# Performance work log

Hardware: AMD Instinct MI355X
Metric: run time of the kernel (lower is better)

## Reference

```python
import jax, jax.numpy as jnp
import numpy as np

B, N, D = 4, 1024, 512
H, Dv, Dq = 8, 64, 64
NUM_BUCKETS = 64
LN_EPS = 1e-5


def setup_inputs() -> dict:
    key = jax.random.key(0)
    ks = jax.random.split(key, 10)
    x = jax.random.normal(ks[0], (B, N, D), dtype=jnp.float32)
    ts = jnp.sort(jax.random.randint(ks[1], (B, N), 0, 1_000_000), axis=1).astype(jnp.int64)
    cm = jnp.triu(jnp.ones((N, N), dtype=bool), k=1)  # causal: mask j > i
    pm = jnp.zeros((B, N), dtype=bool)                # no padding
    uvqk = 0.02 * jax.random.normal(ks[2], (D, 2 * H * Dv + 2 * H * Dq), dtype=jnp.float32)
    lim = float(np.sqrt(6.0 / (H * Dv + D)))
    o_w = jax.random.uniform(ks[3], (H * Dv, D), minval=-lim, maxval=lim, dtype=jnp.float32)
    o_b = jnp.zeros((D,), dtype=jnp.float32)
    ln_x_w = jnp.ones((D,), jnp.float32); ln_x_b = jnp.zeros((D,), jnp.float32)
    ln_a_w = jnp.ones((H * Dv,), jnp.float32); ln_a_b = jnp.zeros((H * Dv,), jnp.float32)
    ts_w = 0.02 * jax.random.normal(ks[4], (NUM_BUCKETS + 1,), dtype=jnp.float32)
    pos_w = 0.02 * jax.random.normal(ks[5], (2 * N - 1,), dtype=jnp.float32)
    return {"x": x, "ts": ts, "cm": cm, "pm": pm, "uvqk": uvqk, "o_w": o_w, "o_b": o_b,
            "ln_x_w": ln_x_w, "ln_x_b": ln_x_b, "ln_a_w": ln_a_w, "ln_a_b": ln_a_b,
            "ts_w": ts_w, "pos_w": pos_w}


def _layernorm(x, w, b):
    m = jnp.mean(x, axis=-1, keepdims=True)
    v = jnp.mean(jnp.square(x - m), axis=-1, keepdims=True)
    return (x - m) / jnp.sqrt(v + LN_EPS) * w + b


def _rel_bias(ts, ts_w, pos_w):
    # positional part: pb[i, j] = pos_w[j - i + N - 1], shape [N, N]
    idx = jnp.arange(N)
    pb = pos_w[idx[None, :] - idx[:, None] + N - 1]
    # bucketed time part
    ext = jnp.concatenate([ts, ts[:, N - 1:N]], axis=1)           # [B, N+1]
    diff = ext[:, 1:, None] - ext[:, None, :-1]                   # [B, N, N]
    logd = jnp.log(jnp.maximum(jnp.abs(diff), 1).astype(jnp.float32))
    bk = jnp.clip((logd / 0.301).astype(jnp.int32), 0, NUM_BUCKETS)
    return pb[None] + ts_w[bk]                                    # [B, N, N]


def reference(x, ts, cm, pm, uvqk, o_w, o_b, ln_x_w, ln_x_b, ln_a_w, ln_a_b, ts_w, pos_w):
    nx = _layernorm(x, ln_x_w, ln_x_b)                            # [B, N, D]
    out = jax.nn.silu(jnp.einsum('bnd,de->bne', nx, uvqk))        # [B, N, 2HDv+2HDq]
    u, v, q, k = jnp.split(out, [H * Dv, 2 * H * Dv, 2 * H * Dv + H * Dq], axis=-1)
    q = q.reshape(B, N, H, Dq)
    k = k.reshape(B, N, H, Dq)
    v = v.reshape(B, N, H, Dv)
    qk = jnp.einsum('bihd,bjhd->bhij', q, k) + _rel_bias(ts, ts_w, pos_w)[:, None]
    qk = jax.nn.silu(qk) / N
    qk = jnp.where(cm[None, None], 0.0, qk)          # causal mask
    qk = jnp.where(pm[:, None, None, :], 0.0, qk)    # padding mask on keys
    ao = jnp.einsum('bhij,bjhd->bihd', qk, v).reshape(B, N, H * Dv)
    ao = _layernorm(ao, ln_a_w, ln_a_b)
    u = u.reshape(B, N, H * Dv)
    y = (u * ao) @ o_w + o_b + x
    return jnp.where(pm[:, :, None], 0.0, y)
```

## Files before the change

kernel.cpp:

```cpp
#include <hip/hip_runtime.h>


typedef __attribute__((ext_vector_type(8))) short short8;
typedef __attribute__((ext_vector_type(4))) short bf4;
typedef __attribute__((ext_vector_type(4))) float floatx4;

#define MFMA_BF16 __builtin_amdgcn_mfma_f32_16x16x32_bf16

static __device__ __forceinline__ short f2bf(float f) {
  unsigned u = __builtin_bit_cast(unsigned, f);
  u = (u + 0x7fffu + ((u >> 16) & 1u)) >> 16;
  return (short)u;
}
static __device__ __forceinline__ float bf2f(short s) {
  unsigned u = ((unsigned)(unsigned short)s) << 16;
  return __builtin_bit_cast(float, u);
}
static __device__ __forceinline__ float silu_f(float x) {
  return x / (1.f + __expf(-x));
}
static __device__ __forceinline__ void gl_lds16(const void* g, void* l) {
  __builtin_amdgcn_global_load_lds(
      (const __attribute__((address_space(1))) unsigned int*)g,
      (__attribute__((address_space(3))) unsigned int*)l, 16, 0, 0);
}

__global__ __launch_bounds__(256) void prep_kernel(
    const float* __restrict__ x, const int* __restrict__ ts,
    const float* __restrict__ uvqk, const float* __restrict__ o_w,
    const float* __restrict__ ln_x_w, const float* __restrict__ ln_x_b,
    const float* __restrict__ ts_w, const float* __restrict__ pos_w,
    short* __restrict__ nx, short* __restrict__ uvqk_t,
    short* __restrict__ o_wt, short* __restrict__ bias) {
  __shared__ float tile[32][33];
  const int id = blockIdx.x;
  const int t = threadIdx.x;
  if (id < 4096) {
    const int b = id >> 10, i = id & 1023;
    int ie = i + 1; if (ie > 1023) ie = 1023;
    const int tse = ts[(b << 10) + ie];
    const int j0 = t * 4;
    int4 tj = *(const int4*)&ts[(b << 10) + j0];
    const int* tjp = (const int*)&tj;
    bf4 o;
#pragma unroll
    for (int e = 0; e < 4; ++e) {
      int dt = tse - tjp[e];
      float ad = fabsf((float)dt);
      if (ad < 1.f) ad = 1.f;
      int bkt = (int)(__logf(ad) * (1.f / 0.301f));
      if (bkt > 64) bkt = 64;
      o[e] = f2bf(pos_w[j0 + e - i + 1023] + ts_w[bkt]);
    }
    *(bf4*)&bias[((size_t)id << 10) + j0] = o;
  } else if (id < 5120) {
    const int lane = t & 63;
    const int row = ((id - 4096) << 2) + (t >> 6);
    const int c0 = lane * 8;
    const float* xr = x + (size_t)row * 512;
    float v[8];
    *(float4*)&v[0] = *(const float4*)(xr + c0);
    *(float4*)&v[4] = *(const float4*)(xr + c0 + 4);
    float s = 0.f, sq = 0.f;
#pragma unroll
    for (int e = 0; e < 8; ++e) { s += v[e]; sq += v[e] * v[e]; }
#pragma unroll
    for (int off = 32; off > 0; off >>= 1) {
      s += __shfl_xor(s, off);
      sq += __shfl_xor(sq, off);
    }
    float m = s * (1.f / 512.f);
    float var = sq * (1.f / 512.f) - m * m;
    float rinv = rsqrtf(var + 1e-5f);
    float wv[8], bv[8];
    *(float4*)&wv[0] = *(const float4*)(ln_x_w + c0);
    *(float4*)&wv[4] = *(const float4*)(ln_x_w + c0 + 4);
    *(float4*)&bv[0] = *(const float4*)(ln_x_b + c0);
    *(float4*)&bv[4] = *(const float4*)(ln_x_b + c0 + 4);
    short8 o;
#pragma unroll
    for (int e = 0; e < 8; ++e) o[e] = f2bf((v[e] - m) * rinv * wv[e] + bv[e]);
    *(short8*)(nx + (size_t)row * 512 + c0) = o;
  } else {
    const float* src; short* dst; int R, C, bc, br;
    if (id < 6144) {
      int idm = id - 5120;
      src = uvqk; dst = uvqk_t; R = 512; C = 2048;
      bc = (idm & 63) * 32; br = (idm >> 6) * 32;
    } else {
      int idm = id - 6144;
      src = o_w; dst = o_wt; R = 512; C = 512;
      bc = (idm & 15) * 32; br = (idm >> 4) * 32;
    }
    const int c = t & 31, r0 = t >> 5;
#pragma unroll
    for (int p = 0; p < 4; ++p) {
      int r = r0 + p * 8;
      tile[r][c] = src[(size_t)(br + r) * C + bc + c];
    }
    __syncthreads();
#pragma unroll
    for (int p = 0; p < 4; ++p) {
      int r = r0 + p * 8;
      dst[(size_t)(bc + r) * R + br + c] = f2bf(tile[c][r]);
    }
  }
}

__global__ __launch_bounds__(256) void gemm1_kernel(
    const short* __restrict__ A, const short* __restrict__ Bt,
    short* __restrict__ u_buf, short* __restrict__ vt_buf,
    short* __restrict__ q_buf, short* __restrict__ k_buf) {
  __shared__ __align__(16) short As[2][128 * 32];
  __shared__ __align__(16) short Bs[2][128 * 32];
  const int t = threadIdx.x;
  const int lane = t & 63, w = t >> 6;
  const int quad = lane >> 4, l15 = lane & 15;
  const int m0 = blockIdx.x * 128, n0 = blockIdx.y * 128;
  const int wm = (w & 1) * 64, wn = (w >> 1) * 64;
  const int lr = lane >> 2, lc = (lane & 3) * 8;
  floatx4 acc[4][4];
#pragma unroll
  for (int i = 0; i < 4; ++i)
#pragma unroll
    for (int j = 0; j < 4; ++j) acc[i][j] = (floatx4){0.f, 0.f, 0.f, 0.f};

  for (int k0 = 0; k0 < 512; k0 += 64) {
    __syncthreads();
#pragma unroll
    for (int c = 0; c < 2; ++c)
#pragma unroll
      for (int p = 0; p < 2; ++p) {
        int ra = w * 32 + p * 16;
        gl_lds16(&A[(size_t)(m0 + ra + lr) * 512 + k0 + c * 32 + lc], &As[c][ra * 32]);
        gl_lds16(&Bt[(size_t)(n0 + ra + lr) * 512 + k0 + c * 32 + lc], &Bs[c][ra * 32]);
      }
    __syncthreads();
#pragma unroll
    for (int c = 0; c < 2; ++c) {
      short8 af[4], bfr[4];
#pragma unroll
      for (int mi = 0; mi < 4; ++mi) af[mi] = *(const short8*)&As[c][(wm + mi * 16 + l15) * 32 + quad * 8];
#pragma unroll
      for (int ni = 0; ni < 4; ++ni) bfr[ni] = *(const short8*)&Bs[c][(wn + ni * 16 + l15) * 32 + quad * 8];
#pragma unroll
      for (int mi = 0; mi < 4; ++mi)
#pragma unroll
        for (int ni = 0; ni < 4; ++ni)
          acc[mi][ni] = MFMA_BF16(af[mi], bfr[ni], acc[mi][ni], 0, 0, 0);
    }
  }
  const int seg = n0 >> 9, cbase = n0 & 511;
  if (seg == 0) {
#pragma unroll
    for (int mi = 0; mi < 4; ++mi)
#pragma unroll
      for (int ni = 0; ni < 4; ++ni)
#pragma unroll
        for (int r = 0; r < 4; ++r) {
          int row = m0 + wm + mi * 16 + quad * 4 + r;
          int c = cbase + wn + ni * 16 + l15;
          u_buf[(size_t)row * 512 + c] = f2bf(silu_f(acc[mi][ni][r]));
        }
  } else if (seg == 1) {
#pragma unroll
    for (int mi = 0; mi < 4; ++mi)
#pragma unroll
      for (int ni = 0; ni < 4; ++ni) {
        int c = cbase + wn + ni * 16 + l15;
        int h = c >> 6, d = c & 63;
        int row0 = m0 + wm + mi * 16 + quad * 4;
        int b_ = row0 >> 10, nb = row0 & 1023;
        bf4 sv;
#pragma unroll
        for (int r = 0; r < 4; ++r) sv[r] = f2bf(silu_f(acc[mi][ni][r]));
        *(bf4*)&vt_buf[(((size_t)(b_ * 8 + h) * 64 + d) << 10) + nb] = sv;
      }
  } else {
    short* dst = (seg == 2) ? q_buf : k_buf;
#pragma unroll
    for (int mi = 0; mi < 4; ++mi)
#pragma unroll
      for (int ni = 0; ni < 4; ++ni)
#pragma unroll
        for (int r = 0; r < 4; ++r) {
          int row = m0 + wm + mi * 16 + quad * 4 + r;
          int c = cbase + wn + ni * 16 + l15;
          int b_ = row >> 10, nseq = row & 1023;
          size_t idx = ((((size_t)(b_ * 8 + (c >> 6))) << 10) + nseq) * 64 + (c & 63);
          dst[idx] = f2bf(silu_f(acc[mi][ni][r]));
        }
  }
}

__global__ __launch_bounds__(256, 4) void attn_kernel(
    const short* __restrict__ q_buf, const short* __restrict__ k_buf,
    const short* __restrict__ vt_buf, const short* __restrict__ bias_buf,
    short* __restrict__ ao_part) {
  __shared__ __align__(16) short q_s[64][72];
  __shared__ __align__(16) short k_s[64][72];
  __shared__ __align__(16) short vt_s[64][72];
  __shared__ __align__(16) short p_s[64][72];

  const int t = threadIdx.x;
  const int lane = t & 63, w = t >> 6;
  const int quad = lane >> 4, l15 = lane & 15;
  const int bh = blockIdx.x, pair = blockIdx.y, jh = blockIdx.z;
  const int b = bh >> 3, h = bh & 7;
  const short* qh = q_buf + (size_t)bh * 65536;
  const short* kh = k_buf + (size_t)bh * 65536;
  const short* vth = vt_buf + (size_t)bh * 65536;
  const int sr = t >> 2, sc = (t & 3) * 16;

#pragma unroll
  for (int half = 0; half < 2; ++half) {
    const int it = half ? (15 - pair) : pair;
    const int i0 = it * 64;
    {
      float4 qr0 = *(const float4*)&qh[(size_t)(i0 + sr) * 64 + sc];
      float4 qr1 = *(const float4*)&qh[(size_t)(i0 + sr) * 64 + sc + 8];
      *(float4*)&q_s[sr][sc] = qr0;
      *(float4*)&q_s[sr][sc + 8] = qr1;
    }
    float4 kr0, kr1, vr0, vr1;
    if (jh <= it) {
      int j0 = jh * 64;
      kr0 = *(const float4*)&kh[(size_t)(j0 + sr) * 64 + sc];
      kr1 = *(const float4*)&kh[(size_t)(j0 + sr) * 64 + sc + 8];
      vr0 = *(const float4*)&vth[(size_t)sr * 1024 + j0 + sc];
      vr1 = *(const float4*)&vth[(size_t)sr * 1024 + j0 + sc + 8];
    }
    floatx4 ao0 = {0.f, 0.f, 0.f, 0.f}, ao1 = ao0, ao2 = ao0, ao3 = ao0;
    for (int jt = jh; jt <= it; jt += 4) {
      const int j0 = jt * 64;
      short br[4][4];
      {
        const short* bb = &bias_buf[((size_t)(b * 1024 + i0 + w * 16 + quad * 4) << 10) + j0 + l15];
#pragma unroll
        for (int ni = 0; ni < 4; ++ni)
#pragma unroll
          for (int r2 = 0; r2 < 4; ++r2)
            br[ni][r2] = bb[((size_t)r2 << 10) + ni * 16];
      }
      __syncthreads();
      *(float4*)&k_s[sr][sc] = kr0;
      *(float4*)&k_s[sr][sc + 8] = kr1;
      *(float4*)&vt_s[sr][sc] = vr0;
      *(float4*)&vt_s[sr][sc + 8] = vr1;
      {
        int jn = (jt + 4 <= it) ? jt + 4 : jt;
        int jn0 = jn * 64;
        kr0 = *(const float4*)&kh[(size_t)(jn0 + sr) * 64 + sc];
        kr1 = *(const float4*)&kh[(size_t)(jn0 + sr) * 64 + sc + 8];
        vr0 = *(const float4*)&vth[(size_t)sr * 1024 + jn0 + sc];
        vr1 = *(const float4*)&vth[(size_t)sr * 1024 + jn0 + sc + 8];
      }
      __syncthreads();
      floatx4 s0 = {0.f, 0.f, 0.f, 0.f}, s1 = s0, s2 = s0, s3 = s0;
#pragma unroll
      for (int kk = 0; kk < 64; kk += 32) {
        short8 aq = *(const short8*)&q_s[w * 16 + l15][kk + quad * 8];
        s0 = MFMA_BF16(aq, *(const short8*)&k_s[0 + l15][kk + quad * 8], s0, 0, 0, 0);
        s1 = MFMA_BF16(aq, *(const short8*)&k_s[16 + l15][kk + quad * 8], s1, 0, 0, 0);
        s2 = MFMA_BF16(aq, *(const short8*)&k_s[32 + l15][kk + quad * 8], s2, 0, 0, 0);
        s3 = MFMA_BF16(aq, *(const short8*)&k_s[48 + l15][kk + quad * 8], s3, 0, 0, 0);
      }
      const bool diag = (jt == it);
      floatx4 sv[4] = {s0, s1, s2, s3};
#pragma unroll
      for (int ni = 0; ni < 4; ++ni) {
        int j_loc = ni * 16 + l15;
#pragma unroll
        for (int r2 = 0; r2 < 4; ++r2) {
          int i_loc = w * 16 + quad * 4 + r2;
          float xx = sv[ni][r2] + bf2f(br[ni][r2]);
          float pv = silu_f(xx) * (1.f / 1024.f);
          if (diag && j_loc > i_loc) pv = 0.f;
          p_s[i_loc][j_loc] = f2bf(pv);
        }
      }
#pragma unroll
      for (int kk = 0; kk < 64; kk += 32) {
        short8 ap = *(const short8*)&p_s[w * 16 + l15][kk + quad * 8];
        ao0 = MFMA_BF16(ap, *(const short8*)&vt_s[0 + l15][kk + quad * 8], ao0, 0, 0, 0);
        ao1 = MFMA_BF16(ap, *(const short8*)&vt_s[16 + l15][kk + quad * 8], ao1, 0, 0, 0);
        ao2 = MFMA_BF16(ap, *(const short8*)&vt_s[32 + l15][kk + quad * 8], ao2, 0, 0, 0);
        ao3 = MFMA_BF16(ap, *(const short8*)&vt_s[48 + l15][kk + quad * 8], ao3, 0, 0, 0);
      }
    }
    floatx4 aov[4] = {ao0, ao1, ao2, ao3};
    short* aod = ao_part + (size_t)jh * 2097152;
#pragma unroll
    for (int ni = 0; ni < 4; ++ni)
#pragma unroll
      for (int r2 = 0; r2 < 4; ++r2) {
        int gi = i0 + w * 16 + quad * 4 + r2;
        int d = ni * 16 + l15;
        aod[((size_t)(b * 1024 + gi)) * 512 + h * 64 + d] = f2bf(aov[ni][r2]);
      }
  }
}

__global__ __launch_bounds__(256) void ln_mul_kernel(
    const short* __restrict__ ao_part, const short* __restrict__ u,
    const float* __restrict__ w_, const float* __restrict__ b_,
    short* __restrict__ g) {
  const int lane = threadIdx.x & 63;
  const int row = (blockIdx.x << 2) + (threadIdx.x >> 6);
  const int c0 = lane * 8;
  short8 a0 = *(const short8*)(ao_part + (size_t)row * 512 + c0);
  short8 a1 = *(const short8*)(ao_part + 2097152 + (size_t)row * 512 + c0);
  short8 a2 = *(const short8*)(ao_part + 4194304 + (size_t)row * 512 + c0);
  short8 a3 = *(const short8*)(ao_part + 6291456 + (size_t)row * 512 + c0);
  float v[8];
#pragma unroll
  for (int e = 0; e < 8; ++e)
    v[e] = (bf2f(a0[e]) + bf2f(a1[e])) + (bf2f(a2[e]) + bf2f(a3[e]));
  float s = 0.f, sq = 0.f;
#pragma unroll
  for (int e = 0; e < 8; ++e) { s += v[e]; sq += v[e] * v[e]; }
#pragma unroll
  for (int off = 32; off > 0; off >>= 1) {
    s += __shfl_xor(s, off);
    sq += __shfl_xor(sq, off);
  }
  float m = s * (1.f / 512.f);
  float var = sq * (1.f / 512.f) - m * m;
  float rinv = rsqrtf(var + 1e-5f);
  float wv[8], bv[8];
  *(float4*)&wv[0] = *(const float4*)(w_ + c0);
  *(float4*)&wv[4] = *(const float4*)(w_ + c0 + 4);
  *(float4*)&bv[0] = *(const float4*)(b_ + c0);
  *(float4*)&bv[4] = *(const float4*)(b_ + c0 + 4);
  short8 uv = *(const short8*)(u + (size_t)row * 512 + c0);
  short8 o;
#pragma unroll
  for (int e = 0; e < 8; ++e)
    o[e] = f2bf(bf2f(uv[e]) * ((v[e] - m) * rinv * wv[e] + bv[e]));
  *(short8*)(g + (size_t)row * 512 + c0) = o;
}

__global__ __launch_bounds__(256) void gemm2_kernel(
    const short* __restrict__ G, const short* __restrict__ Wt,
    const float* __restrict__ o_b, const float* __restrict__ x,
    float* __restrict__ out) {
  __shared__ __align__(16) short As[2][64 * 32];
  __shared__ __align__(16) short Bs[2][64 * 32];
  const int t = threadIdx.x;
  const int lane = t & 63, w = t >> 6;
  const int quad = lane >> 4, l15 = lane & 15;
  const int m0 = blockIdx.x * 64, n0 = blockIdx.y * 64;
  const int lr = lane >> 2, lc = (lane & 3) * 8;
  floatx4 acc[4];
#pragma unroll
  for (int j = 0; j < 4; ++j) acc[j] = (floatx4){0.f, 0.f, 0.f, 0.f};

  for (int k0 = 0; k0 < 512; k0 += 64) {
    __syncthreads();
#pragma unroll
    for (int c = 0; c < 2; ++c) {
      int ra = w * 16;
      gl_lds16(&G[(size_t)(m0 + ra + lr) * 512 + k0 + c * 32 + lc], &As[c][ra * 32]);
      gl_lds16(&Wt[(size_t)(n0 + ra + lr) * 512 + k0 + c * 32 + lc], &Bs[c][ra * 32]);
    }
    __syncthreads();
#pragma unroll
    for (int c = 0; c < 2; ++c) {
      short8 af = *(const short8*)&As[c][(w * 16 + l15) * 32 + quad * 8];
#pragma unroll
      for (int ni = 0; ni < 4; ++ni) {
        short8 bfr = *(const short8*)&Bs[c][(ni * 16 + l15) * 32 + quad * 8];
        acc[ni] = MFMA_BF16(af, bfr, acc[ni], 0, 0, 0);
      }
    }
  }
#pragma unroll
  for (int ni = 0; ni < 4; ++ni)
#pragma unroll
    for (int r = 0; r < 4; ++r) {
      int row = m0 + w * 16 + quad * 4 + r;
      int c = n0 + ni * 16 + l15;
      out[(size_t)row * 512 + c] = acc[ni][r] + o_b[c] + x[(size_t)row * 512 + c];
    }
}

extern "C" void kernel_launch(void* const* d_in, const int* in_sizes, int n_in,
                              void* d_out, int out_size, void* d_ws, size_t ws_size,
                              hipStream_t stream) {
  const float* x = (const float*)d_in[0];
  const int* ts = (const int*)d_in[1];
  const float* uvqk = (const float*)d_in[4];
  const float* o_w = (const float*)d_in[5];
  const float* o_b = (const float*)d_in[6];
  const float* ln_x_w = (const float*)d_in[7];
  const float* ln_x_b = (const float*)d_in[8];
  const float* ln_a_w = (const float*)d_in[9];
  const float* ln_a_b = (const float*)d_in[10];
  const float* ts_w = (const float*)d_in[11];
  const float* pos_w = (const float*)d_in[12];
  float* out = (float*)d_out;

  char* ws = (char*)d_ws;
  short* nx = (short*)(ws + 0);
  short* uvqk_t = (short*)(ws + 4194304);
  short* o_wt = (short*)(ws + 6291456);
  short* u_buf = (short*)(ws + 6815744);
  short* q_buf = (short*)(ws + 11010048);
  short* k_buf = (short*)(ws + 15204352);
  short* vt_buf = (short*)(ws + 19398656);
  short* bias_buf = (short*)(ws + 23592960);
  short* ao_part = (short*)(ws + 31981568);
  short* g_buf = nx;

  hipLaunchKernelGGL(prep_kernel, dim3(6400), dim3(256), 0, stream,
                     x, ts, uvqk, o_w, ln_x_w, ln_x_b, ts_w, pos_w,
                     nx, uvqk_t, o_wt, bias_buf);
  hipLaunchKernelGGL(gemm1_kernel, dim3(32, 16), dim3(256), 0, stream, nx, uvqk_t, u_buf, vt_buf, q_buf, k_buf);
  hipLaunchKernelGGL(attn_kernel, dim3(32, 8, 4), dim3(256), 0, stream, q_buf, k_buf, vt_buf, bias_buf, ao_part);
  hipLaunchKernelGGL(ln_mul_kernel, dim3(1024), dim3(256), 0, stream, ao_part, u_buf, ln_a_w, ln_a_b, g_buf);
  hipLaunchKernelGGL(gemm2_kernel, dim3(64, 8), dim3(256), 0, stream, g_buf, o_wt, o_b, x, out);
}
```

Baseline: 141.5 us.

## Load MFMA operands directly from global memory, dropping LDS staging in GEMMs and attention

Both GEMM kernels stop staging tiles through LDS with global_load_lds and barriers. Each lane now loads its MFMA fragments straight from global memory, with register double-buffering one k-step ahead. The attention kernel likewise reads Q, K and V^T fragments directly into registers, keeping only the P tile in LDS, and drops its occupancy hint from 4 to 3. This removes barriers and LDS traffic but gives up tile reuse across waves, so global/L2 load volume rises and register pressure grows.

```diff
diff --git a/kernel.cpp b/kernel.cpp
--- a/kernel.cpp
+++ b/kernel.cpp
@@ -18,11 +18,6 @@
 }
 static __device__ __forceinline__ float silu_f(float x) {
   return x / (1.f + __expf(-x));
-}
-static __device__ __forceinline__ void gl_lds16(const void* g, void* l) {
-  __builtin_amdgcn_global_load_lds(
-      (const __attribute__((address_space(1))) unsigned int*)g,
-      (__attribute__((address_space(3))) unsigned int*)l, 16, 0, 0);
 }
 
 __global__ __launch_bounds__(256) void prep_kernel(
@@ -111,44 +106,39 @@
     const short* __restrict__ A, const short* __restrict__ Bt,
     short* __restrict__ u_buf, short* __restrict__ vt_buf,
     short* __restrict__ q_buf, short* __restrict__ k_buf) {
-  __shared__ __align__(16) short As[2][128 * 32];
-  __shared__ __align__(16) short Bs[2][128 * 32];
   const int t = threadIdx.x;
   const int lane = t & 63, w = t >> 6;
   const int quad = lane >> 4, l15 = lane & 15;
   const int m0 = blockIdx.x * 128, n0 = blockIdx.y * 128;
   const int wm = (w & 1) * 64, wn = (w >> 1) * 64;
-  const int lr = lane >> 2, lc = (lane & 3) * 8;
+  const short* Ab = A + (size_t)(m0 + wm + l15) * 512 + quad * 8;
+  const short* Bb = Bt + (size_t)(n0 + wn + l15) * 512 + quad * 8;
   floatx4 acc[4][4];
 #pragma unroll
   for (int i = 0; i < 4; ++i)
 #pragma unroll
     for (int j = 0; j < 4; ++j) acc[i][j] = (floatx4){0.f, 0.f, 0.f, 0.f};
 
-  for (int k0 = 0; k0 < 512; k0 += 64) {
-    __syncthreads();
-#pragma unroll
-    for (int c = 0; c < 2; ++c)
-#pragma unroll
-      for (int p = 0; p < 2; ++p) {
-        int ra = w * 32 + p * 16;
-        gl_lds16(&A[(size_t)(m0 + ra + lr) * 512 + k0 + c * 32 + lc], &As[c][ra * 32]);
-        gl_lds16(&Bt[(size_t)(n0 + ra + lr) * 512 + k0 + c * 32 + lc], &Bs[c][ra * 32]);
-      }
-    __syncthreads();
-#pragma unroll
-    for (int c = 0; c < 2; ++c) {
-      short8 af[4], bfr[4];
-#pragma unroll
-      for (int mi = 0; mi < 4; ++mi) af[mi] = *(const short8*)&As[c][(wm + mi * 16 + l15) * 32 + quad * 8];
-#pragma unroll
-      for (int ni = 0; ni < 4; ++ni) bfr[ni] = *(const short8*)&Bs[c][(wn + ni * 16 + l15) * 32 + quad * 8];
-#pragma unroll
-      for (int mi = 0; mi < 4; ++mi)
-#pragma unroll
-        for (int ni = 0; ni < 4; ++ni)
-          acc[mi][ni] = MFMA_BF16(af[mi], bfr[ni], acc[mi][ni], 0, 0, 0);
-    }
+  short8 afc[4], bfc[4], afn[4], bfn[4];
+#pragma unroll
+  for (int mi = 0; mi < 4; ++mi) afc[mi] = *(const short8*)(Ab + mi * 8192);
+#pragma unroll
+  for (int ni = 0; ni < 4; ++ni) bfc[ni] = *(const short8*)(Bb + ni * 8192);
+  for (int k0 = 0; k0 < 512; k0 += 32) {
+    const int kn = (k0 + 32 < 512) ? k0 + 32 : 0;
+#pragma unroll
+    for (int mi = 0; mi < 4; ++mi) afn[mi] = *(const short8*)(Ab + kn + mi * 8192);
+#pragma unroll
+    for (int ni = 0; ni < 4; ++ni) bfn[ni] = *(const short8*)(Bb + kn + ni * 8192);
+#pragma unroll
+    for (int mi = 0; mi < 4; ++mi)
+#pragma unroll
+      for (int ni = 0; ni < 4; ++ni)
+        acc[mi][ni] = MFMA_BF16(afc[mi], bfc[ni], acc[mi][ni], 0, 0, 0);
+#pragma unroll
+    for (int mi = 0; mi < 4; ++mi) afc[mi] = afn[mi];
+#pragma unroll
+    for (int ni = 0; ni < 4; ++ni) bfc[ni] = bfn[ni];
   }
   const int seg = n0 >> 9, cbase = n0 & 511;
   if (seg == 0) {
@@ -193,13 +183,10 @@
   }
 }
 
-__global__ __launch_bounds__(256, 4) void attn_kernel(
+__global__ __launch_bounds__(256, 3) void attn_kernel(
     const short* __restrict__ q_buf, const short* __restrict__ k_buf,
     const short* __restrict__ vt_buf, const short* __restrict__ bias_buf,
     short* __restrict__ ao_part) {
-  __shared__ __align__(16) short q_s[64][72];
-  __shared__ __align__(16) short k_s[64][72];
-  __shared__ __align__(16) short vt_s[64][72];
   __shared__ __align__(16) short p_s[64][72];
 
   const int t = threadIdx.x;
@@ -210,29 +197,29 @@
   const short* qh = q_buf + (size_t)bh * 65536;
   const short* kh = k_buf + (size_t)bh * 65536;
   const short* vth = vt_buf + (size_t)bh * 65536;
-  const int sr = t >> 2, sc = (t & 3) * 16;
 
 #pragma unroll
   for (int half = 0; half < 2; ++half) {
     const int it = half ? (15 - pair) : pair;
     const int i0 = it * 64;
-    {
-      float4 qr0 = *(const float4*)&qh[(size_t)(i0 + sr) * 64 + sc];
-      float4 qr1 = *(const float4*)&qh[(size_t)(i0 + sr) * 64 + sc + 8];
-      *(float4*)&q_s[sr][sc] = qr0;
-      *(float4*)&q_s[sr][sc + 8] = qr1;
-    }
-    float4 kr0, kr1, vr0, vr1;
-    if (jh <= it) {
-      int j0 = jh * 64;
-      kr0 = *(const float4*)&kh[(size_t)(j0 + sr) * 64 + sc];
-      kr1 = *(const float4*)&kh[(size_t)(j0 + sr) * 64 + sc + 8];
-      vr0 = *(const float4*)&vth[(size_t)sr * 1024 + j0 + sc];
-      vr1 = *(const float4*)&vth[(size_t)sr * 1024 + j0 + sc + 8];
-    }
+    short8 aq0 = *(const short8*)&qh[(size_t)(i0 + w * 16 + l15) * 64 + quad * 8];
+    short8 aq1 = *(const short8*)&qh[(size_t)(i0 + w * 16 + l15) * 64 + 32 + quad * 8];
     floatx4 ao0 = {0.f, 0.f, 0.f, 0.f}, ao1 = ao0, ao2 = ao0, ao3 = ao0;
     for (int jt = jh; jt <= it; jt += 4) {
       const int j0 = jt * 64;
+      short8 bk[2][4], bv[2][4];
+#pragma unroll
+      for (int ni = 0; ni < 4; ++ni) {
+        const short* kp = &kh[(size_t)(j0 + ni * 16 + l15) * 64 + quad * 8];
+        bk[0][ni] = *(const short8*)kp;
+        bk[1][ni] = *(const short8*)(kp + 32);
+      }
+#pragma unroll
+      for (int ni = 0; ni < 4; ++ni) {
+        const short* vp = &vth[(size_t)(ni * 16 + l15) * 1024 + j0 + quad * 8];
+        bv[0][ni] = *(const short8*)vp;
+        bv[1][ni] = *(const short8*)(vp + 32);
+      }
       short br[4][4];
       {
         const short* bb = &bias_buf[((size_t)(b * 1024 + i0 + w * 16 + quad * 4) << 10) + j0 + l15];
@@ -242,51 +229,36 @@
           for (int r2 = 0; r2 < 4; ++r2)
             br[ni][r2] = bb[((size_t)r2 << 10) + ni * 16];
       }
-      __syncthreads();
-      *(float4*)&k_s[sr][sc] = kr0;
-      *(float4*)&k_s[sr][sc + 8] = kr1;
-      *(float4*)&vt_s[sr][sc] = vr0;
-      *(float4*)&vt_s[sr][sc + 8] = vr1;
-      {
-        int jn = (jt + 4 <= it) ? jt + 4 : jt;
-        int jn0 = jn * 64;
-        kr0 = *(const float4*)&kh[(size_t)(jn0 + sr) * 64 + sc];
-        kr1 = *(const float4*)&kh[(size_t)(jn0 + sr) * 64 + sc + 8];
-        vr0 = *(const float4*)&vth[(size_t)sr * 1024 + jn0 + sc];
-        vr1 = *(const float4*)&vth[(size_t)sr * 1024 + jn0 + sc + 8];
-      }
-      __syncthreads();
-      floatx4 s0 = {0.f, 0.f, 0.f, 0.f}, s1 = s0, s2 = s0, s3 = s0;
-#pragma unroll
-      for (int kk = 0; kk < 64; kk += 32) {
-        short8 aq = *(const short8*)&q_s[w * 16 + l15][kk + quad * 8];
-        s0 = MFMA_BF16(aq, *(const short8*)&k_s[0 + l15][kk + quad * 8], s0, 0, 0, 0);
-        s1 = MFMA_BF16(aq, *(const short8*)&k_s[16 + l15][kk + quad * 8], s1, 0, 0, 0);
-        s2 = MFMA_BF16(aq, *(const short8*)&k_s[32 + l15][kk + quad * 8], s2, 0, 0, 0);
-        s3 = MFMA_BF16(aq, *(const short8*)&k_s[48 + l15][kk + quad * 8], s3, 0, 0, 0);
+      floatx4 s[4];
+#pragma unroll
+      for (int ni = 0; ni < 4; ++ni) {
+        floatx4 z = {0.f, 0.f, 0.f, 0.f};
+        z = MFMA_BF16(aq0, bk[0][ni], z, 0, 0, 0);
+        s[ni] = MFMA_BF16(aq1, bk[1][ni], z, 0, 0, 0);
       }
       const bool diag = (jt == it);
-      floatx4 sv[4] = {s0, s1, s2, s3};
 #pragma unroll
       for (int ni = 0; ni < 4; ++ni) {
         int j_loc = ni * 16 + l15;
 #pragma unroll
         for (int r2 = 0; r2 < 4; ++r2) {
           int i_loc = w * 16 + quad * 4 + r2;
-          float xx = sv[ni][r2] + bf2f(br[ni][r2]);
+          float xx = s[ni][r2] + bf2f(br[ni][r2]);
           float pv = silu_f(xx) * (1.f / 1024.f);
           if (diag && j_loc > i_loc) pv = 0.f;
           p_s[i_loc][j_loc] = f2bf(pv);
         }
       }
-#pragma unroll
-      for (int kk = 0; kk < 64; kk += 32) {
-        short8 ap = *(const short8*)&p_s[w * 16 + l15][kk + quad * 8];
-        ao0 = MFMA_BF16(ap, *(const short8*)&vt_s[0 + l15][kk + quad * 8], ao0, 0, 0, 0);
-        ao1 = MFMA_BF16(ap, *(const short8*)&vt_s[16 + l15][kk + quad * 8], ao1, 0, 0, 0);
-        ao2 = MFMA_BF16(ap, *(const short8*)&vt_s[32 + l15][kk + quad * 8], ao2, 0, 0, 0);
-        ao3 = MFMA_BF16(ap, *(const short8*)&vt_s[48 + l15][kk + quad * 8], ao3, 0, 0, 0);
-      }
+      short8 ap0 = *(const short8*)&p_s[w * 16 + l15][quad * 8];
+      short8 ap1 = *(const short8*)&p_s[w * 16 + l15][32 + quad * 8];
+      ao0 = MFMA_BF16(ap0, bv[0][0], ao0, 0, 0, 0);
+      ao0 = MFMA_BF16(ap1, bv[1][0], ao0, 0, 0, 0);
+      ao1 = MFMA_BF16(ap0, bv[0][1], ao1, 0, 0, 0);
+      ao1 = MFMA_BF16(ap1, bv[1][1], ao1, 0, 0, 0);
+      ao2 = MFMA_BF16(ap0, bv[0][2], ao2, 0, 0, 0);
+      ao2 = MFMA_BF16(ap1, bv[1][2], ao2, 0, 0, 0);
+      ao3 = MFMA_BF16(ap0, bv[0][3], ao3, 0, 0, 0);
+      ao3 = MFMA_BF16(ap1, bv[1][3], ao3, 0, 0, 0);
     }
     floatx4 aov[4] = {ao0, ao1, ao2, ao3};
     short* aod = ao_part + (size_t)jh * 2097152;
@@ -344,35 +316,31 @@
     const short* __restrict__ G, const short* __restrict__ Wt,
     const float* __restrict__ o_b, const float* __restrict__ x,
     float* __restrict__ out) {
-  __shared__ __align__(16) short As[2][64 * 32];
-  __shared__ __align__(16) short Bs[2][64 * 32];
   const int t = threadIdx.x;
   const int lane = t & 63, w = t >> 6;
   const int quad = lane >> 4, l15 = lane & 15;
   const int m0 = blockIdx.x * 64, n0 = blockIdx.y * 64;
-  const int lr = lane >> 2, lc = (lane & 3) * 8;
+  const short* Ab = G + (size_t)(m0 + w * 16 + l15) * 512 + quad * 8;
+  const short* Bb = Wt + (size_t)(n0 + l15) * 512 + quad * 8;
   floatx4 acc[4];
 #pragma unroll
   for (int j = 0; j < 4; ++j) acc[j] = (floatx4){0.f, 0.f, 0.f, 0.f};
 
-  for (int k0 = 0; k0 < 512; k0 += 64) {
-    __syncthreads();
-#pragma unroll
-    for (int c = 0; c < 2; ++c) {
-      int ra = w * 16;
-      gl_lds16(&G[(size_t)(m0 + ra + lr) * 512 + k0 + c * 32 + lc], &As[c][ra * 32]);
-      gl_lds16(&Wt[(size_t)(n0 + ra + lr) * 512 + k0 + c * 32 + lc], &Bs[c][ra * 32]);
-    }
-    __syncthreads();
-#pragma unroll
-    for (int c = 0; c < 2; ++c) {
-      short8 af = *(const short8*)&As[c][(w * 16 + l15) * 32 + quad * 8];
-#pragma unroll
-      for (int ni = 0; ni < 4; ++ni) {
-        short8 bfr = *(const short8*)&Bs[c][(ni * 16 + l15) * 32 + quad * 8];
-        acc[ni] = MFMA_BF16(af, bfr, acc[ni], 0, 0, 0);
-      }
-    }
+  short8 afc, bfc[4], afn, bfn[4];
+  afc = *(const short8*)Ab;
+#pragma unroll
+  for (int ni = 0; ni < 4; ++ni) bfc[ni] = *(const short8*)(Bb + ni * 8192);
+  for (int k0 = 0; k0 < 512; k0 += 32) {
+    const int kn = (k0 + 32 < 512) ? k0 + 32 : 0;
+    afn = *(const short8*)(Ab + kn);
+#pragma unroll
+    for (int ni = 0; ni < 4; ++ni) bfn[ni] = *(const short8*)(Bb + kn + ni * 8192);
+#pragma unroll
+    for (int ni = 0; ni < 4; ++ni)
+      acc[ni] = MFMA_BF16(afc, bfc[ni], acc[ni], 0, 0, 0);
+    afc = afn;
+#pragma unroll
+    for (int ni = 0; ni < 4; ++ni) bfc[ni] = bfn[ni];
   }
 #pragma unroll
   for (int ni = 0; ni < 4; ++ni)
```

After: 194.4 us. 1.37x slower.

## Use packed bf16 conversion, fold bias into MFMA accumulator, move 1/N scale into V

Applied to the files above, without the earlier changes.

Replaces the manual per-element float-to-bf16 rounding with the packed hardware conversion (__float22bfloat162_rn) in every kernel epilogue. In the attention kernel the relative bias now initializes the QK MFMA accumulators, which removes a separate add. The 1/N scale moves out of the P computation and into V at projection time. This trims VALU work in the conversion-heavy epilogues and in the attention inner loop. Scaling V by 1/1024 before bf16 rounding shifts only the exponent, so precision is essentially unchanged.

```diff
diff --git a/kernel.cpp b/kernel.cpp
--- a/kernel.cpp
+++ b/kernel.cpp
@@ -1,4 +1,5 @@
 #include <hip/hip_runtime.h>
+#include <hip/hip_bf16.h>
 
 
 typedef __attribute__((ext_vector_type(8))) short short8;
@@ -12,6 +13,14 @@
   u = (u + 0x7fffu + ((u >> 16) & 1u)) >> 16;
   return (short)u;
 }
+static __device__ __forceinline__ unsigned pk_bf16(float a, float b) {
+  __hip_bfloat162 h = __float22bfloat162_rn(float2{a, b});
+  unsigned u;
+  __builtin_memcpy(&u, &h, 4);
+  return u;
+}
+static __device__ __forceinline__ short lo16(unsigned u) { return (short)(u & 0xffffu); }
+static __device__ __forceinline__ short hi16(unsigned u) { return (short)(u >> 16); }
 static __device__ __forceinline__ float bf2f(short s) {
   unsigned u = ((unsigned)(unsigned short)s) << 16;
   return __builtin_bit_cast(float, u);
@@ -42,7 +51,7 @@
     const int j0 = t * 4;
     int4 tj = *(const int4*)&ts[(b << 10) + j0];
     const int* tjp = (const int*)&tj;
-    bf4 o;
+    float ov[4];
 #pragma unroll
     for (int e = 0; e < 4; ++e) {
       int dt = tse - tjp[e];
@@ -50,9 +59,10 @@
       if (ad < 1.f) ad = 1.f;
       int bkt = (int)(__logf(ad) * (1.f / 0.301f));
       if (bkt > 64) bkt = 64;
-      o[e] = f2bf(pos_w[j0 + e - i + 1023] + ts_w[bkt]);
-    }
-    *(bf4*)&bias[((size_t)id << 10) + j0] = o;
+      ov[e] = pos_w[j0 + e - i + 1023] + ts_w[bkt];
+    }
+    uint2 o2 = {pk_bf16(ov[0], ov[1]), pk_bf16(ov[2], ov[3])};
+    *(uint2*)&bias[((size_t)id << 10) + j0] = o2;
   } else if (id < 5120) {
     const int lane = t & 63;
     const int row = ((id - 4096) << 2) + (t >> 6);
@@ -77,10 +87,12 @@
     *(float4*)&wv[4] = *(const float4*)(ln_x_w + c0 + 4);
     *(float4*)&bv[0] = *(const float4*)(ln_x_b + c0);
     *(float4*)&bv[4] = *(const float4*)(ln_x_b + c0 + 4);
-    short8 o;
-#pragma unroll
-    for (int e = 0; e < 8; ++e) o[e] = f2bf((v[e] - m) * rinv * wv[e] + bv[e]);
-    *(short8*)(nx + (size_t)row * 512 + c0) = o;
+    float o[8];
+#pragma unroll
+    for (int e = 0; e < 8; ++e) o[e] = (v[e] - m) * rinv * wv[e] + bv[e];
+    uint4 o4 = {pk_bf16(o[0], o[1]), pk_bf16(o[2], o[3]),
+                pk_bf16(o[4], o[5]), pk_bf16(o[6], o[7])};
+    *(uint4*)(nx + (size_t)row * 512 + c0) = o4;
   } else {
     const float* src; short* dst; int R, C, bc, br;
     if (id < 6144) {
@@ -155,13 +167,17 @@
 #pragma unroll
     for (int mi = 0; mi < 4; ++mi)
 #pragma unroll
-      for (int ni = 0; ni < 4; ++ni)
-#pragma unroll
-        for (int r = 0; r < 4; ++r) {
-          int row = m0 + wm + mi * 16 + quad * 4 + r;
-          int c = cbase + wn + ni * 16 + l15;
-          u_buf[(size_t)row * 512 + c] = f2bf(silu_f(acc[mi][ni][r]));
-        }
+      for (int ni = 0; ni < 4; ++ni) {
+        int row0 = m0 + wm + mi * 16 + quad * 4;
+        int c = cbase + wn + ni * 16 + l15;
+        float v0 = silu_f(acc[mi][ni][0]), v1 = silu_f(acc[mi][ni][1]);
+        float v2 = silu_f(acc[mi][ni][2]), v3 = silu_f(acc[mi][ni][3]);
+        unsigned pa = pk_bf16(v0, v1), pb = pk_bf16(v2, v3);
+        u_buf[(size_t)row0 * 512 + c] = lo16(pa);
+        u_buf[(size_t)(row0 + 1) * 512 + c] = hi16(pa);
+        u_buf[(size_t)(row0 + 2) * 512 + c] = lo16(pb);
+        u_buf[(size_t)(row0 + 3) * 512 + c] = hi16(pb);
+      }
   } else if (seg == 1) {
 #pragma unroll
     for (int mi = 0; mi < 4; ++mi)
@@ -171,25 +187,31 @@
         int h = c >> 6, d = c & 63;
         int row0 = m0 + wm + mi * 16 + quad * 4;
         int b_ = row0 >> 10, nb = row0 & 1023;
-        bf4 sv;
-#pragma unroll
-        for (int r = 0; r < 4; ++r) sv[r] = f2bf(silu_f(acc[mi][ni][r]));
-        *(bf4*)&vt_buf[(((size_t)(b_ * 8 + h) * 64 + d) << 10) + nb] = sv;
+        float v0 = silu_f(acc[mi][ni][0]) * (1.f / 1024.f);
+        float v1 = silu_f(acc[mi][ni][1]) * (1.f / 1024.f);
+        float v2 = silu_f(acc[mi][ni][2]) * (1.f / 1024.f);
+        float v3 = silu_f(acc[mi][ni][3]) * (1.f / 1024.f);
+        uint2 sv = {pk_bf16(v0, v1), pk_bf16(v2, v3)};
+        *(uint2*)&vt_buf[(((size_t)(b_ * 8 + h) * 64 + d) << 10) + nb] = sv;
       }
   } else {
     short* dst = (seg == 2) ? q_buf : k_buf;
 #pragma unroll
     for (int mi = 0; mi < 4; ++mi)
 #pragma unroll
-      for (int ni = 0; ni < 4; ++ni)
-#pragma unroll
-        for (int r = 0; r < 4; ++r) {
-          int row = m0 + wm + mi * 16 + quad * 4 + r;
-          int c = cbase + wn + ni * 16 + l15;
-          int b_ = row >> 10, nseq = row & 1023;
-          size_t idx = ((((size_t)(b_ * 8 + (c >> 6))) << 10) + nseq) * 64 + (c & 63);
-          dst[idx] = f2bf(silu_f(acc[mi][ni][r]));
-        }
+      for (int ni = 0; ni < 4; ++ni) {
+        int row0 = m0 + wm + mi * 16 + quad * 4;
+        int c = cbase + wn + ni * 16 + l15;
+        int b_ = row0 >> 10, nb = row0 & 1023;
+        size_t base = ((((size_t)(b_ * 8 + (c >> 6))) << 10) + nb) * 64 + (c & 63);
+        float v0 = silu_f(acc[mi][ni][0]), v1 = silu_f(acc[mi][ni][1]);
+        float v2 = silu_f(acc[mi][ni][2]), v3 = silu_f(acc[mi][ni][3]);
+        unsigned pa = pk_bf16(v0, v1), pb = pk_bf16(v2, v3);
+        dst[base] = lo16(pa);
+        dst[base + 64] = hi16(pa);
+        dst[base + 128] = lo16(pb);
+        dst[base + 192] = hi16(pb);
+      }
   }
 }
 
@@ -256,7 +278,14 @@
         vr1 = *(const float4*)&vth[(size_t)sr * 1024 + jn0 + sc + 8];
       }
       __syncthreads();
-      floatx4 s0 = {0.f, 0.f, 0.f, 0.f}, s1 = s0, s2 = s0, s3 = s0;
+      floatx4 s0, s1, s2, s3;
+#pragma unroll
+      for (int r2 = 0; r2 < 4; ++r2) {
+        s0[r2] = bf2f(br[0][r2]);
+        s1[r2] = bf2f(br[1][r2]);
+        s2[r2] = bf2f(br[2][r2]);
+        s3[r2] = bf2f(br[3][r2]);
+      }
 #pragma unroll
       for (int kk = 0; kk < 64; kk += 32) {
         short8 aq = *(const short8*)&q_s[w * 16 + l15][kk + quad * 8];
@@ -270,14 +299,19 @@
 #pragma unroll
       for (int ni = 0; ni < 4; ++ni) {
         int j_loc = ni * 16 + l15;
+        float pv[4];
 #pragma unroll
         for (int r2 = 0; r2 < 4; ++r2) {
           int i_loc = w * 16 + quad * 4 + r2;
-          float xx = sv[ni][r2] + bf2f(br[ni][r2]);
-          float pv = silu_f(xx) * (1.f / 1024.f);
-          if (diag && j_loc > i_loc) pv = 0.f;
-          p_s[i_loc][j_loc] = f2bf(pv);
+          float p = silu_f(sv[ni][r2]);
+          pv[r2] = (diag && j_loc > i_loc) ? 0.f : p;
         }
+        unsigned pa = pk_bf16(pv[0], pv[1]), pb = pk_bf16(pv[2], pv[3]);
+        int ib = w * 16 + quad * 4;
+        p_s[ib][j_loc] = lo16(pa);
+        p_s[ib + 1][j_loc] = hi16(pa);
+        p_s[ib + 2][j_loc] = lo16(pb);
+        p_s[ib + 3][j_loc] = hi16(pb);
       }
 #pragma unroll
       for (int kk = 0; kk < 64; kk += 32) {
@@ -291,13 +325,17 @@
     floatx4 aov[4] = {ao0, ao1, ao2, ao3};
     short* aod = ao_part + (size_t)jh * 2097152;
 #pragma unroll
-    for (int ni = 0; ni < 4; ++ni)
-#pragma unroll
-      for (int r2 = 0; r2 < 4; ++r2) {
-        int gi = i0 + w * 16 + quad * 4 + r2;
-        int d = ni * 16 + l15;
-        aod[((size_t)(b * 1024 + gi)) * 512 + h * 64 + d] = f2bf(aov[ni][r2]);
-      }
+    for (int ni = 0; ni < 4; ++ni) {
+      int gi0 = i0 + w * 16 + quad * 4;
+      int d = ni * 16 + l15;
+      unsigned pa = pk_bf16(aov[ni][0], aov[ni][1]);
+      unsigned pb = pk_bf16(aov[ni][2], aov[ni][3]);
+      size_t base = ((size_t)(b * 1024 + gi0)) * 512 + h * 64 + d;
+      aod[base] = lo16(pa);
+      aod[base + 512] = hi16(pa);
+      aod[base + 1024] = lo16(pb);
+      aod[base + 1536] = hi16(pb);
+    }
   }
 }
 
@@ -333,11 +371,13 @@
   *(float4*)&bv[0] = *(const float4*)(b_ + c0);
   *(float4*)&bv[4] = *(const float4*)(b_ + c0 + 4);
   short8 uv = *(const short8*)(u + (size_t)row * 512 + c0);
-  short8 o;
+  float o[8];
 #pragma unroll
   for (int e = 0; e < 8; ++e)
-    o[e] = f2bf(bf2f(uv[e]) * ((v[e] - m) * rinv * wv[e] + bv[e]));
-  *(short8*)(g + (size_t)row * 512 + c0) = o;
+    o[e] = bf2f(uv[e]) * ((v[e] - m) * rinv * wv[e] + bv[e]);
+  uint4 o4 = {pk_bf16(o[0], o[1]), pk_bf16(o[2], o[3]),
+              pk_bf16(o[4], o[5]), pk_bf16(o[6], o[7])};
+  *(uint4*)(g + (size_t)row * 512 + c0) = o4;
 }
 
 __global__ __launch_bounds__(256) void gemm2_kernel(
```

New measurement: 140.3 us. Within noise of the previous version (-0.8%).
